# Optimization experiments

Hardware: AMD Instinct MI355X
Metric: run time of the kernel (lower is better)

## Reference

```python
import jax, jax.numpy as jnp
import numpy as np

N = 8192
IN_F = 128
OUT_F = 128
ALPHA = 0.2  # LeakyReLU negative slope
NEG_INF = -9e15


def setup_inputs() -> dict:
    key = jax.random.key(0)
    k1, k2, k3, k4 = jax.random.split(key, 4)
    h = jax.random.normal(k1, (N, IN_F), dtype=jnp.float32)
    adj = jax.random.randint(k2, (N, N), 0, 2, dtype=jnp.int32)
    # nn.Linear(in, out, bias=False).weight is (out, in); store as (in, out) for h @ W
    W = jax.random.normal(k3, (IN_F, OUT_F), dtype=jnp.float32) * (1.0 / np.sqrt(IN_F))
    # a: (2*out_features, 1), xavier_uniform with gain=1.414
    limit = 1.414 * np.sqrt(6.0 / (2 * OUT_F + 1))
    a = jax.random.uniform(k4, (2 * OUT_F, 1), dtype=jnp.float32, minval=-limit, maxval=limit)
    return {"h": h, "adj": adj, "W": W, "a": a}


def reference(h, adj, W, a):
    Wh = h @ W  # (N, OUT_F)
    a1 = a[:OUT_F, 0]   # score contribution from source node i
    a2 = a[OUT_F:, 0]   # score contribution from target node j
    # e_ij = leakyrelu(Wh_i . a1 + Wh_j . a2) -- avoids the O(N^2 * 2F) concat
    s1 = Wh @ a1  # (N,)
    s2 = Wh @ a2  # (N,)
    e = jax.nn.leaky_relu(s1[:, None] + s2[None, :], negative_slope=ALPHA)  # (N, N)
    masked = jnp.where(adj > 0, e, NEG_INF)
    attention = jax.nn.softmax(masked, axis=1)  # (N, N)
    # dropout is a no-op in eval mode
    h_prime = attention @ Wh  # (N, OUT_F)
    return jax.nn.elu(h_prime)  # concat=True -> ELU
```

## Files before the change

kernel.cpp:

```cpp
#include <hip/hip_runtime.h>
#include <cstdint>
#include <cstddef>


#define NROW 8192
#define FDIM 128

typedef _Float16 f16;
typedef f16 f16x8 __attribute__((ext_vector_type(8)));
typedef float f32x4 __attribute__((ext_vector_type(4)));
typedef float f32x16 __attribute__((ext_vector_type(16)));

#define WS_WHT 0u
#define WS_BP  (2u*1024u*1024u)
#define WS_S12 (4u*1024u*1024u)
#define WS_RC  (WS_S12 + 64u*1024u)
#define WS_EF  (WS_RC + 128u*1024u)
#define WS_M2  (WS_EF + 64u*1024u)
#define WS_PWS (WS_M2 + 4u*1024u)

__global__ __launch_bounds__(256) void k1_wh(const float* __restrict__ h,
                                             const float* __restrict__ W,
                                             f16* __restrict__ WhT,
                                             f16* __restrict__ Bp,
                                             unsigned* __restrict__ M2key) {
  __shared__ float hT[128 * 36];
  const int t = (int)threadIdx.x;
  const int rb = (int)blockIdx.x * 32;
  if (blockIdx.x == 0 && t == 0) *M2key = 0u;
  const f32x4* hv = (const f32x4*)(h + (size_t)rb * FDIM);
#pragma unroll
  for (int i = 0; i < 4; ++i) {
    int fidx = t + i * 256;
    f32x4 v = hv[fidx];
    int e0 = fidx * 4;
    int r = e0 >> 7, k = e0 & 127;
    hT[(k + 0) * 36 + r] = v[0];
    hT[(k + 1) * 36 + r] = v[1];
    hT[(k + 2) * 36 + r] = v[2];
    hT[(k + 3) * 36 + r] = v[3];
  }
  __syncthreads();
  const int f = t & 127, rh = t >> 7;
  f32x4 z = {0.f, 0.f, 0.f, 0.f};
  f32x4 acc0 = z, acc1 = z, acc2 = z, acc3 = z;
  for (int k = 0; k < 128; ++k) {
    float w = W[k * FDIM + f];
    const f32x4* hp = (const f32x4*)(hT + k * 36 + rh * 16);
    acc0 += hp[0] * w;
    acc1 += hp[1] * w;
    acc2 += hp[2] * w;
    acc3 += hp[3] * w;
  }
  union { f16 hx[16]; uint4 u[2]; } pk;
#pragma unroll
  for (int q = 0; q < 4; ++q) {
    pk.hx[0 + q]  = (f16)acc0[q];
    pk.hx[4 + q]  = (f16)acc1[q];
    pk.hx[8 + q]  = (f16)acc2[q];
    pk.hx[12 + q] = (f16)acc3[q];
  }
  uint4* dst = (uint4*)(WhT + (size_t)f * NROW + rb + rh * 16);
  dst[0] = pk.u[0];
  dst[1] = pk.u[1];
  f16* bdst = Bp + ((size_t)((blockIdx.x * 2 + rh) * 4 + (f >> 5)) * 64 + (f & 31)) * 8;
  *(uint4*)bdst = pk.u[0];
  *(uint4*)(bdst + 256) = pk.u[1];
}

__global__ __launch_bounds__(256) void k1b_s(const f16* __restrict__ WhT,
                                             const float* __restrict__ a,
                                             float2* __restrict__ s12,
                                             unsigned* __restrict__ M2key) {
  __shared__ float part[2][4][64];
  const int l = (int)threadIdx.x & 63;
  const int fc = (int)threadIdx.x >> 6;
  const int r = (int)blockIdx.x * 64 + l;
  float s1 = 0.f, s2 = 0.f;
  for (int f = fc * 32; f < fc * 32 + 32; ++f) {
    float w = (float)WhT[(size_t)f * NROW + r];
    s1 = fmaf(w, a[f], s1);
    s2 = fmaf(w, a[128 + f], s2);
  }
  part[0][fc][l] = s1;
  part[1][fc][l] = s2;
  __syncthreads();
  if (fc == 0) {
    s1 = part[0][0][l] + part[0][1][l] + part[0][2][l] + part[0][3][l];
    s2 = part[1][0][l] + part[1][1][l] + part[1][2][l] + part[1][3][l];
    s12[r] = make_float2(s1, s2);
    float mx = s2;
#pragma unroll
    for (int off = 32; off; off >>= 1) mx = fmaxf(mx, __shfl_xor(mx, off, 64));
    if (l == 0) {
      unsigned key = __float_as_uint(mx);
      key = (key & 0x80000000u) ? ~key : (key | 0x80000000u);
      atomicMax(M2key, key);
    }
  }
}

__global__ __launch_bounds__(256) void k1c_prep(const float2* __restrict__ s12,
                                                const unsigned* __restrict__ M2key,
                                                float4* __restrict__ RC,
                                                float2* __restrict__ EF) {
  int j = (int)blockIdx.x * 256 + (int)threadIdx.x;
  unsigned key = *M2key;
  float M2 = (key & 0x80000000u) ? __uint_as_float(key ^ 0x80000000u)
                                 : __uint_as_float(~key);
  float2 s = s12[j];
  float c = s.x + M2;
  c = fmaxf(c, 0.2f * c);
  RC[j] = make_float4(__expf(-s.x), __expf(s.x - c), __expf(0.2f * s.x - c), 0.f);
  EF[j] = make_float2(__expf(s.y), __expf(0.2f * s.y));
}

__global__ __launch_bounds__(256) void k2_main(const int* __restrict__ adj,
                                               const f16* __restrict__ Bp,
                                               const float4* __restrict__ RC,
                                               const float* __restrict__ EF,
                                               float* __restrict__ Pws,
                                               float* __restrict__ Dws,
                                               int jspan) {
  const int tid = (int)threadIdx.x;
  const int L = tid & 63, w = tid >> 6;
  const int wid = (int)blockIdx.x * 4 + w;
  const int rg = wid & 255;
  const int c = wid >> 8;
  const int rb = rg * 32;
  const int m = L & 31, kb = L >> 5;
  const int row = rb + m;
  const int j0 = c * jspan;
  const int niter = jspan >> 5;

  const float4 rc = RC[row];
  const float tau = rc.x, kap1 = rc.y, kap2 = rc.z;

  const int* ap = adj + (size_t)row * NROW + j0 + kb * 8;
  const f32x4* ep = (const f32x4*)(EF + 2 * (j0 + kb * 8));
  const f16* bp = Bp + (size_t)(j0 >> 4) * 2048 + L * 8;

  int4 A0 = *(const int4*)ap;
  int4 A1 = *(const int4*)(ap + 4);
  int4 A2 = *(const int4*)(ap + 16);
  int4 A3 = *(const int4*)(ap + 20);
  f32x4 E0 = ep[0], E1 = ep[1], E2 = ep[2], E3 = ep[3];
  f32x4 E4 = ep[8], E5 = ep[9], E6 = ep[10], E7 = ep[11];

  f32x16 zz = {0.f};
  f32x16 acc[4] = {zz, zz, zz, zz};
  float dloc = 0.f;

  for (int it = 0; it < niter; ++it) {
    const f16* bt = bp + (size_t)it * 4096;
    f16x8 B00 = *(const f16x8*)(bt);
    f16x8 B01 = *(const f16x8*)(bt + 512);
    f16x8 B02 = *(const f16x8*)(bt + 1024);
    f16x8 B03 = *(const f16x8*)(bt + 1536);
    f16x8 B10 = *(const f16x8*)(bt + 2048);
    f16x8 B11 = *(const f16x8*)(bt + 2560);
    f16x8 B12 = *(const f16x8*)(bt + 3072);
    f16x8 B13 = *(const f16x8*)(bt + 3584);

    f16x8 af0, af1;
    {
      float p;
      p = (E0[0] > tau) ? E0[0] * kap1 : E0[1] * kap2; p = (A0.x > 0) ? p : 0.f; dloc += p; af0[0] = (f16)p;
      p = (E0[2] > tau) ? E0[2] * kap1 : E0[3] * kap2; p = (A0.y > 0) ? p : 0.f; dloc += p; af0[1] = (f16)p;
      p = (E1[0] > tau) ? E1[0] * kap1 : E1[1] * kap2; p = (A0.z > 0) ? p : 0.f; dloc += p; af0[2] = (f16)p;
      p = (E1[2] > tau) ? E1[2] * kap1 : E1[3] * kap2; p = (A0.w > 0) ? p : 0.f; dloc += p; af0[3] = (f16)p;
      p = (E2[0] > tau) ? E2[0] * kap1 : E2[1] * kap2; p = (A1.x > 0) ? p : 0.f; dloc += p; af0[4] = (f16)p;
      p = (E2[2] > tau) ? E2[2] * kap1 : E2[3] * kap2; p = (A1.y > 0) ? p : 0.f; dloc += p; af0[5] = (f16)p;
      p = (E3[0] > tau) ? E3[0] * kap1 : E3[1] * kap2; p = (A1.z > 0) ? p : 0.f; dloc += p; af0[6] = (f16)p;
      p = (E3[2] > tau) ? E3[2] * kap1 : E3[3] * kap2; p = (A1.w > 0) ? p : 0.f; dloc += p; af0[7] = (f16)p;
      p = (E4[0] > tau) ? E4[0] * kap1 : E4[1] * kap2; p = (A2.x > 0) ? p : 0.f; dloc += p; af1[0] = (f16)p;
      p = (E4[2] > tau) ? E4[2] * kap1 : E4[3] * kap2; p = (A2.y > 0) ? p : 0.f; dloc += p; af1[1] = (f16)p;
      p = (E5[0] > tau) ? E5[0] * kap1 : E5[1] * kap2; p = (A2.z > 0) ? p : 0.f; dloc += p; af1[2] = (f16)p;
      p = (E5[2] > tau) ? E5[2] * kap1 : E5[3] * kap2; p = (A2.w > 0) ? p : 0.f; dloc += p; af1[3] = (f16)p;
      p = (E6[0] > tau) ? E6[0] * kap1 : E6[1] * kap2; p = (A3.x > 0) ? p : 0.f; dloc += p; af1[4] = (f16)p;
      p = (E6[2] > tau) ? E6[2] * kap1 : E6[3] * kap2; p = (A3.y > 0) ? p : 0.f; dloc += p; af1[5] = (f16)p;
      p = (E7[0] > tau) ? E7[0] * kap1 : E7[1] * kap2; p = (A3.z > 0) ? p : 0.f; dloc += p; af1[6] = (f16)p;
      p = (E7[2] > tau) ? E7[2] * kap1 : E7[3] * kap2; p = (A3.w > 0) ? p : 0.f; dloc += p; af1[7] = (f16)p;
    }

    int adv = (it < niter - 1) ? 1 : 0;
    ap += adv * 32;
    ep += adv * 16;
    A0 = *(const int4*)ap;
    A1 = *(const int4*)(ap + 4);
    A2 = *(const int4*)(ap + 16);
    A3 = *(const int4*)(ap + 20);
    E0 = ep[0]; E1 = ep[1]; E2 = ep[2]; E3 = ep[3];
    E4 = ep[8]; E5 = ep[9]; E6 = ep[10]; E7 = ep[11];

    acc[0] = __builtin_amdgcn_mfma_f32_32x32x16_f16(af0, B00, acc[0], 0, 0, 0);
    acc[1] = __builtin_amdgcn_mfma_f32_32x32x16_f16(af0, B01, acc[1], 0, 0, 0);
    acc[2] = __builtin_amdgcn_mfma_f32_32x32x16_f16(af0, B02, acc[2], 0, 0, 0);
    acc[3] = __builtin_amdgcn_mfma_f32_32x32x16_f16(af0, B03, acc[3], 0, 0, 0);
    acc[0] = __builtin_amdgcn_mfma_f32_32x32x16_f16(af1, B10, acc[0], 0, 0, 0);
    acc[1] = __builtin_amdgcn_mfma_f32_32x32x16_f16(af1, B11, acc[1], 0, 0, 0);
    acc[2] = __builtin_amdgcn_mfma_f32_32x32x16_f16(af1, B12, acc[2], 0, 0, 0);
    acc[3] = __builtin_amdgcn_mfma_f32_32x32x16_f16(af1, B13, acc[3], 0, 0, 0);
  }

  dloc += __shfl_xor(dloc, 32, 64);
  if (L < 32) Dws[(size_t)c * NROW + row] = dloc;

  float* P = Pws + ((size_t)c * NROW + rb) * FDIM + (L & 31);
#pragma unroll
  for (int nt = 0; nt < 4; ++nt) {
#pragma unroll
    for (int reg = 0; reg < 16; ++reg) {
      int rr = (reg & 3) + 8 * (reg >> 2) + 4 * kb;
      P[(size_t)rr * FDIM + nt * 32] = acc[nt][reg];
    }
  }
}

__global__ __launch_bounds__(256) void k3_comb(const float* __restrict__ Pws,
                                               const float* __restrict__ Dws,
                                               float* __restrict__ out, int S) {
  int g = (int)blockIdx.x * 256 + (int)threadIdx.x;
  int r = g >> 5, f4 = g & 31;
  f32x4 s = {0.f, 0.f, 0.f, 0.f};
  float den = 0.f;
  for (int c2 = 0; c2 < S; ++c2) {
    s += *(const f32x4*)(Pws + ((size_t)c2 * NROW + r) * FDIM + f4 * 4);
    den += Dws[(size_t)c2 * NROW + r];
  }
  float inv = 1.0f / den;
  f32x4 o;
#pragma unroll
  for (int e = 0; e < 4; ++e) {
    float x = s[e] * inv;
    o[e] = x > 0.f ? x : expm1f(x);
  }
  *(f32x4*)(out + (size_t)r * FDIM + f4 * 4) = o;
}

extern "C" void kernel_launch(void* const* d_in, const int* in_sizes, int n_in,
                              void* d_out, int out_size, void* d_ws, size_t ws_size,
                              hipStream_t stream) {
  const float* h = (const float*)d_in[0];
  const int* adj = (const int*)d_in[1];
  const float* W = (const float*)d_in[2];
  const float* a = (const float*)d_in[3];
  float* out = (float*)d_out;
  char* ws = (char*)d_ws;
  f16* WhT = (f16*)(ws + WS_WHT);
  f16* Bp = (f16*)(ws + WS_BP);
  float2* s12 = (float2*)(ws + WS_S12);
  float4* RC = (float4*)(ws + WS_RC);
  float2* EF = (float2*)(ws + WS_EF);
  unsigned* M2 = (unsigned*)(ws + WS_M2);

  const size_t partial_bytes = (size_t)NROW * FDIM * 4;
  int S = (ws_size >= WS_PWS + 8 * partial_bytes + 8 * NROW * 4) ? 8 : 2;
  float* Pws = (float*)(ws + WS_PWS);
  float* Dws = (float*)(ws + WS_PWS + (size_t)S * partial_bytes);
  int jspan = NROW / S;

  k1_wh<<<dim3(256), dim3(256), 0, stream>>>(h, W, WhT, Bp, M2);
  k1b_s<<<dim3(128), dim3(256), 0, stream>>>(WhT, a, s12, M2);
  k1c_prep<<<dim3(32), dim3(256), 0, stream>>>(s12, M2, RC, EF);
  k2_main<<<dim3(64 * S), dim3(256), 0, stream>>>(adj, Bp, RC, (const float*)EF, Pws, Dws, jspan);
  k3_comb<<<dim3(1024), dim3(256), 0, stream>>>(Pws, Dws, out, S);
}
```

Measured before the change: 450.2 us.

## Pack adjacency matrix into bitmask before main attention kernel

Adds a pre-pass kernel that reads the int32 adjacency matrix once and writes it as a per-row bitmask laid out by 32-row group, using wavefront ballots. The main kernel then reads one 32-bit word per lane per iteration instead of four int4 loads, and tests bits to apply the mask. The full 256 MB adjacency is still read once in the pre-pass, so the gain depends on whether the main kernel was limited by adj traffic or by load latency. The pack pass adds a launch plus an 8 MB write and read.

```diff
diff --git a/kernel.cpp b/kernel.cpp
--- a/kernel.cpp
+++ b/kernel.cpp
@@ -18,6 +18,28 @@
 #define WS_EF  (WS_RC + 128u*1024u)
 #define WS_M2  (WS_EF + 64u*1024u)
 #define WS_PWS (WS_M2 + 4u*1024u)
+
+__global__ __launch_bounds__(256) void k0_pack(const int* __restrict__ adj,
+                                               unsigned* __restrict__ bm) {
+  const int w = (int)threadIdx.x >> 6, l = (int)threadIdx.x & 63;
+  const int r = (int)blockIdx.x * 4 + w;
+  const int rg = r >> 5, m = r & 31;
+  const int* ap = adj + (size_t)r * NROW + l;
+  unsigned* bp = bm + (size_t)rg * (256 * 32) + m;
+  for (int jb = 0; jb < NROW; jb += 128) {
+    int v0 = ap[jb];
+    int v1 = ap[jb + 64];
+    unsigned long long m0 = __ballot(v0 > 0);
+    unsigned long long m1 = __ballot(v1 > 0);
+    if (l == 0) {
+      int jw = jb >> 5;
+      bp[(size_t)(jw + 0) * 32] = (unsigned)m0;
+      bp[(size_t)(jw + 1) * 32] = (unsigned)(m0 >> 32);
+      bp[(size_t)(jw + 2) * 32] = (unsigned)m1;
+      bp[(size_t)(jw + 3) * 32] = (unsigned)(m1 >> 32);
+    }
+  }
+}
 
 __global__ __launch_bounds__(256) void k1_wh(const float* __restrict__ h,
                                              const float* __restrict__ W,
@@ -115,7 +137,7 @@
   EF[j] = make_float2(__expf(s.y), __expf(0.2f * s.y));
 }
 
-__global__ __launch_bounds__(256) void k2_main(const int* __restrict__ adj,
+__global__ __launch_bounds__(256) void k2_main(const unsigned* __restrict__ bm,
                                                const f16* __restrict__ Bp,
                                                const float4* __restrict__ RC,
                                                const float* __restrict__ EF,
@@ -136,14 +158,11 @@
   const float4 rc = RC[row];
   const float tau = rc.x, kap1 = rc.y, kap2 = rc.z;
 
-  const int* ap = adj + (size_t)row * NROW + j0 + kb * 8;
+  const unsigned* wp = bm + ((size_t)rg * 256 + (size_t)(j0 >> 5)) * 32 + m;
   const f32x4* ep = (const f32x4*)(EF + 2 * (j0 + kb * 8));
   const f16* bp = Bp + (size_t)(j0 >> 4) * 2048 + L * 8;
 
-  int4 A0 = *(const int4*)ap;
-  int4 A1 = *(const int4*)(ap + 4);
-  int4 A2 = *(const int4*)(ap + 16);
-  int4 A3 = *(const int4*)(ap + 20);
+  unsigned WD = *wp;
   f32x4 E0 = ep[0], E1 = ep[1], E2 = ep[2], E3 = ep[3];
   f32x4 E4 = ep[8], E5 = ep[9], E6 = ep[10], E7 = ep[11];
 
@@ -162,34 +181,33 @@
     f16x8 B12 = *(const f16x8*)(bt + 3072);
     f16x8 B13 = *(const f16x8*)(bt + 3584);
 
+    const unsigned u0 = WD >> (kb * 8);
+    const unsigned u1 = u0 >> 16;
     f16x8 af0, af1;
     {
       float p;
-      p = (E0[0] > tau) ? E0[0] * kap1 : E0[1] * kap2; p = (A0.x > 0) ? p : 0.f; dloc += p; af0[0] = (f16)p;
-      p = (E0[2] > tau) ? E0[2] * kap1 : E0[3] * kap2; p = (A0.y > 0) ? p : 0.f; dloc += p; af0[1] = (f16)p;
-      p = (E1[0] > tau) ? E1[0] * kap1 : E1[1] * kap2; p = (A0.z > 0) ? p : 0.f; dloc += p; af0[2] = (f16)p;
-      p = (E1[2] > tau) ? E1[2] * kap1 : E1[3] * kap2; p = (A0.w > 0) ? p : 0.f; dloc += p; af0[3] = (f16)p;
-      p = (E2[0] > tau) ? E2[0] * kap1 : E2[1] * kap2; p = (A1.x > 0) ? p : 0.f; dloc += p; af0[4] = (f16)p;
-      p = (E2[2] > tau) ? E2[2] * kap1 : E2[3] * kap2; p = (A1.y > 0) ? p : 0.f; dloc += p; af0[5] = (f16)p;
-      p = (E3[0] > tau) ? E3[0] * kap1 : E3[1] * kap2; p = (A1.z > 0) ? p : 0.f; dloc += p; af0[6] = (f16)p;
-      p = (E3[2] > tau) ? E3[2] * kap1 : E3[3] * kap2; p = (A1.w > 0) ? p : 0.f; dloc += p; af0[7] = (f16)p;
-      p = (E4[0] > tau) ? E4[0] * kap1 : E4[1] * kap2; p = (A2.x > 0) ? p : 0.f; dloc += p; af1[0] = (f16)p;
-      p = (E4[2] > tau) ? E4[2] * kap1 : E4[3] * kap2; p = (A2.y > 0) ? p : 0.f; dloc += p; af1[1] = (f16)p;
-      p = (E5[0] > tau) ? E5[0] * kap1 : E5[1] * kap2; p = (A2.z > 0) ? p : 0.f; dloc += p; af1[2] = (f16)p;
-      p = (E5[2] > tau) ? E5[2] * kap1 : E5[3] * kap2; p = (A2.w > 0) ? p : 0.f; dloc += p; af1[3] = (f16)p;
-      p = (E6[0] > tau) ? E6[0] * kap1 : E6[1] * kap2; p = (A3.x > 0) ? p : 0.f; dloc += p; af1[4] = (f16)p;
-      p = (E6[2] > tau) ? E6[2] * kap1 : E6[3] * kap2; p = (A3.y > 0) ? p : 0.f; dloc += p; af1[5] = (f16)p;
-      p = (E7[0] > tau) ? E7[0] * kap1 : E7[1] * kap2; p = (A3.z > 0) ? p : 0.f; dloc += p; af1[6] = (f16)p;
-      p = (E7[2] > tau) ? E7[2] * kap1 : E7[3] * kap2; p = (A3.w > 0) ? p : 0.f; dloc += p; af1[7] = (f16)p;
+      p = (E0[0] > tau) ? E0[0] * kap1 : E0[1] * kap2; p = (u0 & 1u)   ? p : 0.f; dloc += p; af0[0] = (f16)p;
+      p = (E0[2] > tau) ? E0[2] * kap1 : E0[3] * kap2; p = (u0 & 2u)   ? p : 0.f; dloc += p; af0[1] = (f16)p;
+      p = (E1[0] > tau) ? E1[0] * kap1 : E1[1] * kap2; p = (u0 & 4u)   ? p : 0.f; dloc += p; af0[2] = (f16)p;
+      p = (E1[2] > tau) ? E1[2] * kap1 : E1[3] * kap2; p = (u0 & 8u)   ? p : 0.f; dloc += p; af0[3] = (f16)p;
+      p = (E2[0] > tau) ? E2[0] * kap1 : E2[1] * kap2; p = (u0 & 16u)  ? p : 0.f; dloc += p; af0[4] = (f16)p;
+      p = (E2[2] > tau) ? E2[2] * kap1 : E2[3] * kap2; p = (u0 & 32u)  ? p : 0.f; dloc += p; af0[5] = (f16)p;
+      p = (E3[0] > tau) ? E3[0] * kap1 : E3[1] * kap2; p = (u0 & 64u)  ? p : 0.f; dloc += p; af0[6] = (f16)p;
+      p = (E3[2] > tau) ? E3[2] * kap1 : E3[3] * kap2; p = (u0 & 128u) ? p : 0.f; dloc += p; af0[7] = (f16)p;
+      p = (E4[0] > tau) ? E4[0] * kap1 : E4[1] * kap2; p = (u1 & 1u)   ? p : 0.f; dloc += p; af1[0] = (f16)p;
+      p = (E4[2] > tau) ? E4[2] * kap1 : E4[3] * kap2; p = (u1 & 2u)   ? p : 0.f; dloc += p; af1[1] = (f16)p;
+      p = (E5[0] > tau) ? E5[0] * kap1 : E5[1] * kap2; p = (u1 & 4u)   ? p : 0.f; dloc += p; af1[2] = (f16)p;
+      p = (E5[2] > tau) ? E5[2] * kap1 : E5[3] * kap2; p = (u1 & 8u)   ? p : 0.f; dloc += p; af1[3] = (f16)p;
+      p = (E6[0] > tau) ? E6[0] * kap1 : E6[1] * kap2; p = (u1 & 16u)  ? p : 0.f; dloc += p; af1[4] = (f16)p;
+      p = (E6[2] > tau) ? E6[2] * kap1 : E6[3] * kap2; p = (u1 & 32u)  ? p : 0.f; dloc += p; af1[5] = (f16)p;
+      p = (E7[0] > tau) ? E7[0] * kap1 : E7[1] * kap2; p = (u1 & 64u)  ? p : 0.f; dloc += p; af1[6] = (f16)p;
+      p = (E7[2] > tau) ? E7[2] * kap1 : E7[3] * kap2; p = (u1 & 128u) ? p : 0.f; dloc += p; af1[7] = (f16)p;
     }
 
     int adv = (it < niter - 1) ? 1 : 0;
-    ap += adv * 32;
+    wp += adv * 32;
     ep += adv * 16;
-    A0 = *(const int4*)ap;
-    A1 = *(const int4*)(ap + 4);
-    A2 = *(const int4*)(ap + 16);
-    A3 = *(const int4*)(ap + 20);
+    WD = *wp;
     E0 = ep[0]; E1 = ep[1]; E2 = ep[2]; E3 = ep[3];
     E4 = ep[8]; E5 = ep[9]; E6 = ep[10]; E7 = ep[11];
 
@@ -255,14 +273,17 @@
   unsigned* M2 = (unsigned*)(ws + WS_M2);
 
   const size_t partial_bytes = (size_t)NROW * FDIM * 4;
-  int S = (ws_size >= WS_PWS + 8 * partial_bytes + 8 * NROW * 4) ? 8 : 2;
+  const size_t bm_bytes = (size_t)8 * 1024 * 1024;
+  int S = (ws_size >= WS_PWS + 8 * partial_bytes + 8 * (size_t)NROW * 4 + bm_bytes) ? 8 : 2;
   float* Pws = (float*)(ws + WS_PWS);
   float* Dws = (float*)(ws + WS_PWS + (size_t)S * partial_bytes);
+  unsigned* BM = (unsigned*)(ws + WS_PWS + (size_t)S * partial_bytes + (size_t)S * NROW * 4);
   int jspan = NROW / S;
 
+  k0_pack<<<dim3(2048), dim3(256), 0, stream>>>(adj, BM);
   k1_wh<<<dim3(256), dim3(256), 0, stream>>>(h, W, WhT, Bp, M2);
   k1b_s<<<dim3(128), dim3(256), 0, stream>>>(WhT, a, s12, M2);
   k1c_prep<<<dim3(32), dim3(256), 0, stream>>>(s12, M2, RC, EF);
-  k2_main<<<dim3(64 * S), dim3(256), 0, stream>>>(adj, Bp, RC, (const float*)EF, Pws, Dws, jspan);
+  k2_main<<<dim3(64 * S), dim3(256), 0, stream>>>(BM, Bp, RC, (const float*)EF, Pws, Dws, jspan);
   k3_comb<<<dim3(1024), dim3(256), 0, stream>>>(Pws, Dws, out, S);
 }
```

Result: no change. 452.2 us (+0.4%).
